# Performance work log

Hardware: AMD Instinct MI355X
Metric: run time of the kernel (lower is better)

Reference implementation:

```python
import jax, jax.numpy as jnp
import numpy as np

SEQ = 2048
D_MODEL = 2048
N_HEAD = 16
D_QK = 128
D_V = 128
THETA = 10000.0


def setup_inputs() -> dict:
    key = jax.random.key(0)
    kx, kq, kk, kv, ko = jax.random.split(key, 5)
    x = jax.random.normal(kx, (SEQ, D_MODEL), dtype=jnp.float32)
    q = jax.random.normal(kq, (N_HEAD, D_MODEL, D_QK), dtype=jnp.float32)
    k = jax.random.normal(kk, (N_HEAD, D_MODEL, D_QK), dtype=jnp.float32)
    v = jax.random.normal(kv, (N_HEAD, D_MODEL, D_V), dtype=jnp.float32)
    o = jax.random.normal(ko, (N_HEAD, D_V, D_MODEL), dtype=jnp.float32)
    theta_factor = jnp.asarray(THETA, dtype=jnp.float32)
    return {"x": x, "q": q, "k": k, "v": v, "o": o, "theta_factor": theta_factor}


def _rope_embed(x, d_qk, theta_factor):
    # x: [..., S, d]. Rotate-half RoPE with frequencies theta^(-i/d_rope),
    # then scale by d_qk^(-1/4) so q.k gets the usual 1/sqrt(d_qk).
    S, d = x.shape[-2], x.shape[-1]
    d_rope = d // 2
    rates = theta_factor ** (-jnp.arange(d_rope, dtype=x.dtype) / d_rope)  # [d_rope]
    ang = jnp.arange(S, dtype=x.dtype)[:, None] * rates[None, :]           # [S, d_rope]
    sin, cos = jnp.sin(ang), jnp.cos(ang)
    x1, x2 = x[..., :d_rope], x[..., d_rope:]
    y = jnp.concatenate([cos * x1 - sin * x2, sin * x1 + cos * x2], axis=-1)
    return y * (d_qk ** -0.25)


def reference(x, q, k, v, o, theta_factor):
    # x: [S, D]; q,k: [H, D, d_qk]; v: [H, D, d_v]; o: [H, d_v, D]
    S = x.shape[0]
    d_qk = q.shape[2]
    qs = jnp.einsum('sd,hde->hse', x, q)   # [H, S, d_qk]
    ks = jnp.einsum('sd,hde->hse', x, k)   # [H, S, d_qk]
    vs = jnp.einsum('sd,hde->hse', x, v)   # [H, S, d_v]
    rq = _rope_embed(qs, d_qk, theta_factor)
    rk = _rope_embed(ks, d_qk, theta_factor)
    scores = jnp.einsum('hse,hte->hst', rq, rk)  # [H, S, S]
    causal = jnp.tril(jnp.ones((S, S), dtype=bool))
    scores = jnp.where(causal[None], scores, -jnp.inf)
    w = jax.nn.softmax(scores, axis=-1)
    y = jnp.einsum('hst,hte->hse', w, vs)        # [H, S, d_v]
    z = jnp.einsum('hse,hed->sd', y, o)          # [S, D] (sum over heads)
    return z
```

## Files before the change

### kernel.cpp

```cpp
#include <hip/hip_runtime.h>
#include <hip/hip_bf16.h>

#define SEQ 2048
#define DM  2048
#define NH  16
#define DE  128
#define DR  64
#define LDT 72
#define LDK 136

typedef __attribute__((ext_vector_type(8))) short bf16x8;
typedef __attribute__((ext_vector_type(4))) float f32x4;

__device__ __forceinline__ unsigned short f2bf(float f) {
  unsigned u = __float_as_uint(f);
  u += 0x7fff + ((u >> 16) & 1);
  return (unsigned short)(u >> 16);
}
__device__ __forceinline__ float bf2f(unsigned short h) {
  return __uint_as_float((unsigned)h << 16);
}

__device__ __forceinline__ void gld16(const unsigned short* g, unsigned short* l) {
  __builtin_amdgcn_global_load_lds(
      (const __attribute__((address_space(1))) unsigned int*)g,
      (__attribute__((address_space(3))) unsigned int*)l, 16, 0, 0);
}

__global__ void k_split(const float* __restrict__ in, unsigned short* __restrict__ hi,
                        unsigned short* __restrict__ lo, int n4) {
  int i = blockIdx.x * blockDim.x + threadIdx.x;
  int stride = gridDim.x * blockDim.x;
  for (int idx = i; idx < n4; idx += stride) {
    float4 v = ((const float4*)in)[idx];
    ushort4 h, l;
    h.x = f2bf(v.x); l.x = f2bf(v.x - bf2f(h.x));
    h.y = f2bf(v.y); l.y = f2bf(v.y - bf2f(h.y));
    h.z = f2bf(v.z); l.z = f2bf(v.z - bf2f(h.z));
    h.w = f2bf(v.w); l.w = f2bf(v.w - bf2f(h.w));
    ((ushort4*)hi)[idx] = h;
    ((ushort4*)lo)[idx] = l;
  }
}

__global__ void k_prep_all(const float* __restrict__ q, const float* __restrict__ k,
                           const float* __restrict__ v, const float* __restrict__ o,
                           unsigned short* __restrict__ wqh, unsigned short* __restrict__ wql,
                           unsigned short* __restrict__ wkh, unsigned short* __restrict__ wkl,
                           unsigned short* __restrict__ wvh, unsigned short* __restrict__ otb) {
  __shared__ float tile[32][33];
  int f = blockIdx.x;
  int tx = threadIdx.x, ty = threadIdx.y;
  if (f < 12288) {
    int z = f >> 8;
    int rem = f & 255;
    int ry = rem >> 2, rx = rem & 3;
    int which = z >> 4, h = z & 15;
    const float* in = (which == 0) ? q : (which == 1) ? k : v;
    size_t bo = (size_t)h * DM * DE;
    int r0 = ry * 32, c0 = rx * 32;
    #pragma unroll
    for (int i = 0; i < 32; i += 8)
      tile[ty + i][tx] = in[bo + (size_t)(r0 + ty + i) * DE + (c0 + tx)];
    __syncthreads();
    #pragma unroll
    for (int i = 0; i < 32; i += 8) {
      float vv = tile[tx][ty + i];
      unsigned short hh = f2bf(vv);
      size_t oidx = bo + (size_t)(c0 + ty + i) * DM + (r0 + tx);
      if (which == 0)      { wqh[oidx] = hh; wql[oidx] = f2bf(vv - bf2f(hh)); }
      else if (which == 1) { wkh[oidx] = hh; wkl[oidx] = f2bf(vv - bf2f(hh)); }
      else                 { wvh[oidx] = hh; }
    }
  } else {
    int rem = f - 12288;
    int ry = rem >> 6, rx = rem & 63;
    int r0 = ry * 32, c0 = rx * 32;
    #pragma unroll
    for (int i = 0; i < 32; i += 8)
      tile[ty + i][tx] = o[(size_t)(r0 + ty + i) * DM + (c0 + tx)];
    __syncthreads();
    #pragma unroll
    for (int i = 0; i < 32; i += 8)
      otb[(size_t)(c0 + ty + i) * DM + (r0 + tx)] = f2bf(tile[tx][ty + i]);
  }
}

__global__ void k_rope_tables(const float* __restrict__ theta_p,
                              float* __restrict__ cost, float* __restrict__ sint) {
  int s = blockIdx.x, j = threadIdx.x;
  float theta = theta_p[0];
  float rate = powf(theta, -(float)j * (1.0f / (float)DR));
  float ang = (float)s * rate;
  cost[s * DR + j] = cosf(ang);
  sint[s * DR + j] = sinf(ang);
}

__launch_bounds__(256)
__global__ void k_projall(const unsigned short* __restrict__ xh, const unsigned short* __restrict__ xl,
                          const unsigned short* __restrict__ wqh, const unsigned short* __restrict__ wql,
                          const unsigned short* __restrict__ wkh, const unsigned short* __restrict__ wkl,
                          const unsigned short* __restrict__ wvh,
                          unsigned short* __restrict__ rqh, unsigned short* __restrict__ rql,
                          unsigned short* __restrict__ rkh, unsigned short* __restrict__ rkl,
                          unsigned short* __restrict__ vstt,
                          const float* __restrict__ cost, const float* __restrict__ sint) {
  __shared__ unsigned short Ahs[2][128 * 32];
  __shared__ unsigned short Als[2][128 * 32];
  __shared__ unsigned short Bhs[2][128 * 32];
  __shared__ unsigned short Bls[2][128 * 32];
  int mt = blockIdx.x;
  int mat = blockIdx.y >> 4, h = blockIdx.y & 15;
  bool split = (mat < 2);
  const unsigned short* wph = (mat == 0 ? wqh : (mat == 1 ? wkh : wvh)) + (size_t)h * DE * DM;
  const unsigned short* wpl = (mat == 0 ? wql : wkl) + (size_t)h * DE * DM;
  int m0 = mt * 128;
  int tid = threadIdx.x, lane = tid & 63, wid = tid >> 6;
  int wr = wid >> 1, wc = wid & 1;

  f32x4 zero = {0.f, 0.f, 0.f, 0.f};
  f32x4 acc[4][4];
  #pragma unroll
  for (int i = 0; i < 4; ++i)
    #pragma unroll
    for (int j = 0; j < 4; ++j) acc[i][j] = zero;

  auto STAGE = [&](int buf, int k0) {
    #pragma unroll
    for (int p = 0; p < 2; ++p) {
      int r = p * 64 + wid * 16 + (lane >> 2);
      int c = ((lane & 3) ^ ((r >> 1) & 3)) * 8;
      int ld = r * 32 + (lane & 3) * 8;
      gld16(&xh[(size_t)(m0 + r) * DM + k0 + c], &Ahs[buf][ld]);
      gld16(&wph[(size_t)r * DM + k0 + c], &Bhs[buf][ld]);
      if (split) {
        gld16(&xl[(size_t)(m0 + r) * DM + k0 + c], &Als[buf][ld]);
        gld16(&wpl[(size_t)r * DM + k0 + c], &Bls[buf][ld]);
      }
    }
  };

  const int NT = DM / 32;
  STAGE(0, 0);
  int cl_ = lane & 15;
  int chunk = lane >> 4;
  #pragma unroll 2
  for (int t = 0; t < NT; ++t) {
    int buf = t & 1;
    __syncthreads();
    if (t + 1 < NT) STAGE(buf ^ 1, (t + 1) * 32);
    bf16x8 ah[4], al[4], bh[4], bl[4];
    #pragma unroll
    for (int mf = 0; mf < 4; ++mf) {
      int row = wr * 64 + mf * 16 + cl_;
      int off = row * 32 + ((chunk ^ ((row >> 1) & 3)) * 8);
      ah[mf] = *(const bf16x8*)&Ahs[buf][off];
      if (split) al[mf] = *(const bf16x8*)&Als[buf][off];
    }
    #pragma unroll
    for (int nf = 0; nf < 4; ++nf) {
      int nfi = wc * 2 + (nf & 1) + (nf >> 1) * 4;
      int row = nfi * 16 + cl_;
      int off = row * 32 + ((chunk ^ ((row >> 1) & 3)) * 8);
      bh[nf] = *(const bf16x8*)&Bhs[buf][off];
      if (split) bl[nf] = *(const bf16x8*)&Bls[buf][off];
    }
    if (split) {
      #pragma unroll
      for (int mf = 0; mf < 4; ++mf)
        #pragma unroll
        for (int nf = 0; nf < 4; ++nf) {
          acc[mf][nf] = __builtin_amdgcn_mfma_f32_16x16x32_bf16(ah[mf], bh[nf], acc[mf][nf], 0, 0, 0);
          acc[mf][nf] = __builtin_amdgcn_mfma_f32_16x16x32_bf16(al[mf], bh[nf], acc[mf][nf], 0, 0, 0);
          acc[mf][nf] = __builtin_amdgcn_mfma_f32_16x16x32_bf16(ah[mf], bl[nf], acc[mf][nf], 0, 0, 0);
        }
    } else {
      #pragma unroll
      for (int mf = 0; mf < 4; ++mf)
        #pragma unroll
        for (int nf = 0; nf < 4; ++nf)
          acc[mf][nf] = __builtin_amdgcn_mfma_f32_16x16x32_bf16(ah[mf], bh[nf], acc[mf][nf], 0, 0, 0);
    }
  }

  int cl = lane & 15, rl = (lane >> 4) * 4;
  if (mat == 2) {
    #pragma unroll
    for (int mf = 0; mf < 4; ++mf)
      #pragma unroll
      for (int nf = 0; nf < 4; ++nf) {
        int nfi = wc * 2 + (nf & 1) + (nf >> 1) * 4;
        #pragma unroll
        for (int j = 0; j < 4; ++j) {
          int s = m0 + wr * 64 + mf * 16 + rl + j;
          int e = nfi * 16 + cl;
          vstt[((size_t)h * DE + e) * SEQ + s] = f2bf(acc[mf][nf][j]);
        }
      }
  } else {
    unsigned short* oh = (mat == 0) ? rqh : rkh;
    unsigned short* ol = (mat == 0) ? rql : rkl;
    const float qsc = 0.2973017787506803f;
    #pragma unroll
    for (int mf = 0; mf < 4; ++mf)
      #pragma unroll
      for (int nf = 0; nf < 2; ++nf)
        #pragma unroll
        for (int j = 0; j < 4; ++j) {
          int s = m0 + wr * 64 + mf * 16 + rl + j;
          int e = wc * 32 + (nf & 1) * 16 + cl;
          float x1 = acc[mf][nf][j];
          float x2 = acc[mf][nf + 2][j];
          float c  = cost[s * DR + e];
          float sn = sint[s * DR + e];
          float v1 = (c * x1 - sn * x2) * qsc;
          float v2 = (sn * x1 + c * x2) * qsc;
          size_t i1 = ((size_t)h * SEQ + s) * DE + e;
          size_t i2 = i1 + DR;
          unsigned short h1 = f2bf(v1), h2 = f2bf(v2);
          oh[i1] = h1; ol[i1] = f2bf(v1 - bf2f(h1));
          oh[i2] = h2; ol[i2] = f2bf(v2 - bf2f(h2));
        }
  }
}

#define LOADKV(t0)                                                        \
  pkh0 = *(const int4*)&Kh[(size_t)((t0) + sk_r     ) * DE + sk_c];       \
  pkh1 = *(const int4*)&Kh[(size_t)((t0) + sk_r + 16) * DE + sk_c];       \
  pkh2 = *(const int4*)&Kh[(size_t)((t0) + sk_r + 32) * DE + sk_c];       \
  pkh3 = *(const int4*)&Kh[(size_t)((t0) + sk_r + 48) * DE + sk_c];       \
  pkl0 = *(const int4*)&Kl[(size_t)((t0) + sk_r     ) * DE + sk_c];       \
  pkl1 = *(const int4*)&Kl[(size_t)((t0) + sk_r + 16) * DE + sk_c];       \
  pkl2 = *(const int4*)&Kl[(size_t)((t0) + sk_r + 32) * DE + sk_c];       \
  pkl3 = *(const int4*)&Kl[(size_t)((t0) + sk_r + 48) * DE + sk_c];       \
  pvv0 = *(const int4*)&Vt[(size_t)(sv_r     ) * SEQ + (t0) + sv_c];      \
  pvv1 = *(const int4*)&Vt[(size_t)(sv_r + 32) * SEQ + (t0) + sv_c];      \
  pvv2 = *(const int4*)&Vt[(size_t)(sv_r + 64) * SEQ + (t0) + sv_c];      \
  pvv3 = *(const int4*)&Vt[(size_t)(sv_r + 96) * SEQ + (t0) + sv_c];

#define STOREKV()                                                         \
  *(int4*)&Khi[(sk_r     ) * LDK + sk_c] = pkh0;                          \
  *(int4*)&Khi[(sk_r + 16) * LDK + sk_c] = pkh1;                          \
  *(int4*)&Khi[(sk_r + 32) * LDK + sk_c] = pkh2;                          \
  *(int4*)&Khi[(sk_r + 48) * LDK + sk_c] = pkh3;                          \
  *(int4*)&Klo[(sk_r     ) * LDK + sk_c] = pkl0;                          \
  *(int4*)&Klo[(sk_r + 16) * LDK + sk_c] = pkl1;                          \
  *(int4*)&Klo[(sk_r + 32) * LDK + sk_c] = pkl2;                          \
  *(int4*)&Klo[(sk_r + 48) * LDK + sk_c] = pkl3;                          \
  *(int4*)&Vtl[(sv_r     ) * LDT + sv_c] = pvv0;                          \
  *(int4*)&Vtl[(sv_r + 32) * LDT + sv_c] = pvv1;                          \
  *(int4*)&Vtl[(sv_r + 64) * LDT + sv_c] = pvv2;                          \
  *(int4*)&Vtl[(sv_r + 96) * LDT + sv_c] = pvv3;

__launch_bounds__(256, 2)
__global__ void k_attn(const unsigned short* __restrict__ rqh, const unsigned short* __restrict__ rql,
                       const unsigned short* __restrict__ rkh, const unsigned short* __restrict__ rkl,
                       const unsigned short* __restrict__ vstt,
                       unsigned short* __restrict__ yb) {
  __shared__ unsigned short Khi[64 * LDK];
  __shared__ unsigned short Klo[64 * LDK];
  __shared__ unsigned short Vtl[128 * LDT];
  __shared__ unsigned short Pl[64 * LDT];
  int bid = blockIdx.x;
  int g = bid >> 4;
  int qt = (g < 16) ? (31 - g) : (g - 16);
  int h  = bid & 15;
  int m0 = qt * 64;
  int tid = threadIdx.x, lane = tid & 63, wid = tid >> 6;
  const unsigned short* Qh = rqh + (size_t)h * SEQ * DE;
  const unsigned short* Ql = rql + (size_t)h * SEQ * DE;
  const unsigned short* Kh = rkh + (size_t)h * SEQ * DE;
  const unsigned short* Kl = rkl + (size_t)h * SEQ * DE;
  const unsigned short* Vt = vstt + (size_t)h * DE * SEQ;
  int cl = lane & 15, hi = lane >> 4;

  bf16x8 qfh[4], qfl[4];
  {
    int qrow = m0 + wid * 16 + cl;
    #pragma unroll
    for (int ks = 0; ks < 4; ++ks) {
      qfh[ks] = *(const bf16x8*)&Qh[(size_t)qrow * DE + ks * 32 + hi * 8];
      qfl[ks] = *(const bf16x8*)&Ql[(size_t)qrow * DE + ks * 32 + hi * 8];
    }
  }

  f32x4 zero = {0.f, 0.f, 0.f, 0.f};
  f32x4 acc[8];
  #pragma unroll
  for (int nf = 0; nf < 8; ++nf) acc[nf] = zero;
  float mrow[4], lrow[4];
  #pragma unroll
  for (int j = 0; j < 4; ++j) { mrow[j] = -3e38f; lrow[j] = 0.f; }

  int sk_r = tid >> 4, sk_c = (tid & 15) * 8;
  int sv_r = tid >> 3, sv_c = (tid & 7) * 8;

  int4 pkh0, pkh1, pkh2, pkh3, pkl0, pkl1, pkl2, pkl3, pvv0, pvv1, pvv2, pvv3;

  int ntiles = qt + 1;
  LOADKV(0)
  for (int t = 0; t < ntiles; ++t) {
    int t0 = t * 64;
    STOREKV()
    __syncthreads();
    if (t + 1 < ntiles) { LOADKV(t0 + 64) }

    f32x4 sacc[4];
    #pragma unroll
    for (int tf = 0; tf < 4; ++tf) sacc[tf] = zero;
    __builtin_amdgcn_s_setprio(1);
    #pragma unroll
    for (int ks = 0; ks < 4; ++ks) {
      int kk = ks * 32 + hi * 8;
      #pragma unroll
      for (int tf = 0; tf < 4; ++tf) {
        int r = (tf * 16 + cl) * LDK + kk;
        bf16x8 bh = *(const bf16x8*)&Khi[r];
        bf16x8 bl = *(const bf16x8*)&Klo[r];
        sacc[tf] = __builtin_amdgcn_mfma_f32_16x16x32_bf16(qfh[ks], bh, sacc[tf], 0, 0, 0);
        sacc[tf] = __builtin_amdgcn_mfma_f32_16x16x32_bf16(qfl[ks], bh, sacc[tf], 0, 0, 0);
        sacc[tf] = __builtin_amdgcn_mfma_f32_16x16x32_bf16(qfh[ks], bl, sacc[tf], 0, 0, 0);
      }
    }
    __builtin_amdgcn_s_setprio(0);
    if (t == ntiles - 1) {
      int sb = m0 + wid * 16 + hi * 4;
      #pragma unroll
      for (int tf = 0; tf < 4; ++tf) {
        int tc = t0 + tf * 16 + cl;
        #pragma unroll
        for (int j = 0; j < 4; ++j)
          if (tc > sb + j) sacc[tf][j] = -3e38f;
      }
    }
    float mxa[4];
    #pragma unroll
    for (int j = 0; j < 4; ++j) {
      float mx = fmaxf(fmaxf(sacc[0][j], sacc[1][j]), fmaxf(sacc[2][j], sacc[3][j]));
      mx = fmaxf(mx, __shfl_xor(mx, 1));
      mx = fmaxf(mx, __shfl_xor(mx, 2));
      mx = fmaxf(mx, __shfl_xor(mx, 4));
      mx = fmaxf(mx, __shfl_xor(mx, 8));
      mxa[j] = mx;
    }
    bool need = (mxa[0] > mrow[0] + 8.f) || (mxa[1] > mrow[1] + 8.f) ||
                (mxa[2] > mrow[2] + 8.f) || (mxa[3] > mrow[3] + 8.f);
    if (__any(need)) {
      #pragma unroll
      for (int j = 0; j < 4; ++j) {
        float mnew = fmaxf(mrow[j], mxa[j]);
        float sc = __expf(mrow[j] - mnew);
        float sum = 0.f;
        #pragma unroll
        for (int tf = 0; tf < 4; ++tf) {
          float p = __expf(sacc[tf][j] - mnew);
          sacc[tf][j] = p;
          sum += p;
        }
        sum += __shfl_xor(sum, 1);
        sum += __shfl_xor(sum, 2);
        sum += __shfl_xor(sum, 4);
        sum += __shfl_xor(sum, 8);
        lrow[j] = lrow[j] * sc + sum;
        mrow[j] = mnew;
        #pragma unroll
        for (int nf = 0; nf < 8; ++nf) acc[nf][j] *= sc;
      }
    } else {
      #pragma unroll
      for (int j = 0; j < 4; ++j) {
        float sum = 0.f;
        #pragma unroll
        for (int tf = 0; tf < 4; ++tf) {
          float p = __expf(sacc[tf][j] - mrow[j]);
          sacc[tf][j] = p;
          sum += p;
        }
        sum += __shfl_xor(sum, 1);
        sum += __shfl_xor(sum, 2);
        sum += __shfl_xor(sum, 4);
        sum += __shfl_xor(sum, 8);
        lrow[j] += sum;
      }
    }
    #pragma unroll
    for (int tf = 0; tf < 4; ++tf)
      #pragma unroll
      for (int j = 0; j < 4; ++j)
        Pl[(wid * 16 + hi * 4 + j) * LDT + tf * 16 + cl] = f2bf(sacc[tf][j]);
    __builtin_amdgcn_s_setprio(1);
    #pragma unroll
    for (int ks = 0; ks < 2; ++ks) {
      int kk = ks * 32 + hi * 8;
      bf16x8 a = *(const bf16x8*)&Pl[(wid * 16 + cl) * LDT + kk];
      #pragma unroll
      for (int nf = 0; nf < 8; ++nf) {
        bf16x8 b = *(const bf16x8*)&Vtl[(nf * 16 + cl) * LDT + kk];
        acc[nf] = __builtin_amdgcn_mfma_f32_16x16x32_bf16(a, b, acc[nf], 0, 0, 0);
      }
    }
    __builtin_amdgcn_s_setprio(0);
    __syncthreads();
  }

  #pragma unroll
  for (int j = 0; j < 4; ++j) {
    float inv = 1.0f / lrow[j];
    #pragma unroll
    for (int nf = 0; nf < 8; ++nf) acc[nf][j] *= inv;
  }
  #pragma unroll
  for (int nf = 0; nf < 8; ++nf)
    #pragma unroll
    for (int j = 0; j < 4; ++j) {
      int s = m0 + wid * 16 + hi * 4 + j;
      int e = nf * 16 + cl;
      yb[(size_t)s * DM + h * DE + e] = f2bf(acc[nf][j]);
    }
}

__launch_bounds__(256)
__global__ void k_out(const unsigned short* __restrict__ yb,
                      const unsigned short* __restrict__ otb,
                      float* __restrict__ z) {
  __shared__ unsigned short Ahs[2][128 * 32];
  __shared__ unsigned short Bhs[2][128 * 32];
  int m0 = blockIdx.x * 128, n0 = blockIdx.y * 128;
  int tid = threadIdx.x, lane = tid & 63, wid = tid >> 6;
  int wr = wid >> 1, wc = wid & 1;
  f32x4 zero = {0.f, 0.f, 0.f, 0.f};
  f32x4 acc[4][4];
  #pragma unroll
  for (int i = 0; i < 4; ++i)
    #pragma unroll
    for (int j = 0; j < 4; ++j) acc[i][j] = zero;

  auto STAGE = [&](int buf, int k0) {
    #pragma unroll
    for (int p = 0; p < 2; ++p) {
      int r = p * 64 + wid * 16 + (lane >> 2);
      int c = ((lane & 3) ^ ((r >> 1) & 3)) * 8;
      int ld = r * 32 + (lane & 3) * 8;
      gld16(&yb[(size_t)(m0 + r) * DM + k0 + c], &Ahs[buf][ld]);
      gld16(&otb[(size_t)(n0 + r) * DM + k0 + c], &Bhs[buf][ld]);
    }
  };

  const int NT = DM / 32;
  STAGE(0, 0);
  int cl_ = lane & 15;
  int chunk = lane >> 4;
  #pragma unroll 2
  for (int t = 0; t < NT; ++t) {
    int buf = t & 1;
    __syncthreads();
    if (t + 1 < NT) STAGE(buf ^ 1, (t + 1) * 32);
    bf16x8 a[4], b[4];
    #pragma unroll
    for (int mf = 0; mf < 4; ++mf) {
      int row = wr * 64 + mf * 16 + cl_;
      a[mf] = *(const bf16x8*)&Ahs[buf][row * 32 + ((chunk ^ ((row >> 1) & 3)) * 8)];
    }
    #pragma unroll
    for (int nf = 0; nf < 4; ++nf) {
      int nfi = wc * 2 + (nf & 1) + (nf >> 1) * 4;
      int row = nfi * 16 + cl_;
      b[nf] = *(const bf16x8*)&Bhs[buf][row * 32 + ((chunk ^ ((row >> 1) & 3)) * 8)];
    }
    #pragma unroll
    for (int mf = 0; mf < 4; ++mf)
      #pragma unroll
      for (int nf = 0; nf < 4; ++nf)
        acc[mf][nf] = __builtin_amdgcn_mfma_f32_16x16x32_bf16(a[mf], b[nf], acc[mf][nf], 0, 0, 0);
  }
  int cl = lane & 15, rl = (lane >> 4) * 4;
  #pragma unroll
  for (int mf = 0; mf < 4; ++mf)
    #pragma unroll
    for (int nf = 0; nf < 4; ++nf) {
      int nfi = wc * 2 + (nf & 1) + (nf >> 1) * 4;
      #pragma unroll
      for (int j = 0; j < 4; ++j) {
        int s = m0 + wr * 64 + mf * 16 + rl + j;
        int d = n0 + nfi * 16 + cl;
        z[(size_t)s * DM + d] = acc[mf][nf][j];
      }
    }
}

extern "C" void kernel_launch(void* const* d_in, const int* in_sizes, int n_in,
                              void* d_out, int out_size, void* d_ws, size_t ws_size,
                              hipStream_t stream) {
  const float* x  = (const float*)d_in[0];
  const float* q  = (const float*)d_in[1];
  const float* k  = (const float*)d_in[2];
  const float* v  = (const float*)d_in[3];
  const float* o  = (const float*)d_in[4];
  const float* th = (const float*)d_in[5];
  float* z = (float*)d_out;
  char* ws = (char*)d_ws;
  const size_t MB = 1024 * 1024;
  unsigned short* xh  = (unsigned short*)(ws);
  unsigned short* xl  = (unsigned short*)(ws + 8 * MB);
  unsigned short* wqh = (unsigned short*)(ws + 16 * MB);
  unsigned short* wql = (unsigned short*)(ws + 24 * MB);
  unsigned short* wkh = (unsigned short*)(ws + 32 * MB);
  unsigned short* wkl = (unsigned short*)(ws + 40 * MB);
  unsigned short* wvh = (unsigned short*)(ws + 48 * MB);
  unsigned short* rqh = (unsigned short*)(ws + 56 * MB);
  unsigned short* rql = (unsigned short*)(ws + 64 * MB);
  unsigned short* rkh = (unsigned short*)(ws + 72 * MB);
  unsigned short* rkl = (unsigned short*)(ws + 80 * MB);
  unsigned short* vst = (unsigned short*)(ws + 88 * MB);
  float* cost = (float*)(ws + 96 * MB);
  float* sint = (float*)(ws + 96 * MB + 512 * 1024);
  unsigned short* otb = (unsigned short*)(ws + 98 * MB);
  unsigned short* yb  = (unsigned short*)(ws + 16 * MB);

  dim3 tb(32, 8);
  k_rope_tables<<<SEQ, DR, 0, stream>>>(th, cost, sint);
  k_split<<<2048, 256, 0, stream>>>(x, xh, xl, SEQ * DM / 4);
  k_prep_all<<<16384, tb, 0, stream>>>(q, k, v, o, wqh, wql, wkh, wkl, wvh, otb);
  k_projall<<<dim3(16, 48), 256, 0, stream>>>(xh, xl, wqh, wql, wkh, wkl, wvh,
                                              rqh, rql, rkh, rkl, vst, cost, sint);
  k_attn<<<512, 256, 0, stream>>>(rqh, rql, rkh, rkl, vst, yb);
  k_out<<<dim3(16, 16), 256, 0, stream>>>(yb, otb, z);
}
```

Before: 312.3 us.

## Shrink attention tiles to 32 rows with 2-wave blocks and interleave heads

The attention kernel now uses 32-query by 32-key tiles with 128-thread blocks (two waves) and launches twice as many blocks. Shared-memory buffers and strides are resized to match, and the head index is permuted across block IDs. The goal is better load balance and occupancy across CUs for the causal triangular workload. In exchange, each key/value byte is reused by fewer query rows, so more tile loads and barriers are needed per unit of work.

New measurement: 324.9 us. +4.0%, slower.

```diff
diff --git a/kernel.cpp b/kernel.cpp
--- a/kernel.cpp
+++ b/kernel.cpp
@@ -6,8 +6,9 @@
 #define NH  16
 #define DE  128
 #define DR  64
-#define LDT 72
 #define LDK 136
+#define LDV 36
+#define LDP 36
 
 typedef __attribute__((ext_vector_type(8))) short bf16x8;
 typedef __attribute__((ext_vector_type(4))) float f32x4;
@@ -226,13 +227,13 @@
 
 #define LOADKV(t0)                                                        \
   pkh0 = *(const int4*)&Kh[(size_t)((t0) + sk_r     ) * DE + sk_c];       \
-  pkh1 = *(const int4*)&Kh[(size_t)((t0) + sk_r + 16) * DE + sk_c];       \
-  pkh2 = *(const int4*)&Kh[(size_t)((t0) + sk_r + 32) * DE + sk_c];       \
-  pkh3 = *(const int4*)&Kh[(size_t)((t0) + sk_r + 48) * DE + sk_c];       \
+  pkh1 = *(const int4*)&Kh[(size_t)((t0) + sk_r +  8) * DE + sk_c];       \
+  pkh2 = *(const int4*)&Kh[(size_t)((t0) + sk_r + 16) * DE + sk_c];       \
+  pkh3 = *(const int4*)&Kh[(size_t)((t0) + sk_r + 24) * DE + sk_c];       \
   pkl0 = *(const int4*)&Kl[(size_t)((t0) + sk_r     ) * DE + sk_c];       \
-  pkl1 = *(const int4*)&Kl[(size_t)((t0) + sk_r + 16) * DE + sk_c];       \
-  pkl2 = *(const int4*)&Kl[(size_t)((t0) + sk_r + 32) * DE + sk_c];       \
-  pkl3 = *(const int4*)&Kl[(size_t)((t0) + sk_r + 48) * DE + sk_c];       \
+  pkl1 = *(const int4*)&Kl[(size_t)((t0) + sk_r +  8) * DE + sk_c];       \
+  pkl2 = *(const int4*)&Kl[(size_t)((t0) + sk_r + 16) * DE + sk_c];       \
+  pkl3 = *(const int4*)&Kl[(size_t)((t0) + sk_r + 24) * DE + sk_c];       \
   pvv0 = *(const int4*)&Vt[(size_t)(sv_r     ) * SEQ + (t0) + sv_c];      \
   pvv1 = *(const int4*)&Vt[(size_t)(sv_r + 32) * SEQ + (t0) + sv_c];      \
   pvv2 = *(const int4*)&Vt[(size_t)(sv_r + 64) * SEQ + (t0) + sv_c];      \
@@ -240,32 +241,32 @@
 
 #define STOREKV()                                                         \
   *(int4*)&Khi[(sk_r     ) * LDK + sk_c] = pkh0;                          \
-  *(int4*)&Khi[(sk_r + 16) * LDK + sk_c] = pkh1;                          \
-  *(int4*)&Khi[(sk_r + 32) * LDK + sk_c] = pkh2;                          \
-  *(int4*)&Khi[(sk_r + 48) * LDK + sk_c] = pkh3;                          \
+  *(int4*)&Khi[(sk_r +  8) * LDK + sk_c] = pkh1;                          \
+  *(int4*)&Khi[(sk_r + 16) * LDK + sk_c] = pkh2;                          \
+  *(int4*)&Khi[(sk_r + 24) * LDK + sk_c] = pkh3;                          \
   *(int4*)&Klo[(sk_r     ) * LDK + sk_c] = pkl0;                          \
-  *(int4*)&Klo[(sk_r + 16) * LDK + sk_c] = pkl1;                          \
-  *(int4*)&Klo[(sk_r + 32) * LDK + sk_c] = pkl2;                          \
-  *(int4*)&Klo[(sk_r + 48) * LDK + sk_c] = pkl3;                          \
-  *(int4*)&Vtl[(sv_r     ) * LDT + sv_c] = pvv0;                          \
-  *(int4*)&Vtl[(sv_r + 32) * LDT + sv_c] = pvv1;                          \
-  *(int4*)&Vtl[(sv_r + 64) * LDT + sv_c] = pvv2;                          \
-  *(int4*)&Vtl[(sv_r + 96) * LDT + sv_c] = pvv3;
-
-__launch_bounds__(256, 2)
+  *(int4*)&Klo[(sk_r +  8) * LDK + sk_c] = pkl1;                          \
+  *(int4*)&Klo[(sk_r + 16) * LDK + sk_c] = pkl2;                          \
+  *(int4*)&Klo[(sk_r + 24) * LDK + sk_c] = pkl3;                          \
+  *(int4*)&Vtl[(sv_r     ) * LDV + sv_c] = pvv0;                          \
+  *(int4*)&Vtl[(sv_r + 32) * LDV + sv_c] = pvv1;                          \
+  *(int4*)&Vtl[(sv_r + 64) * LDV + sv_c] = pvv2;                          \
+  *(int4*)&Vtl[(sv_r + 96) * LDV + sv_c] = pvv3;
+
+__launch_bounds__(128, 2)
 __global__ void k_attn(const unsigned short* __restrict__ rqh, const unsigned short* __restrict__ rql,
                        const unsigned short* __restrict__ rkh, const unsigned short* __restrict__ rkl,
                        const unsigned short* __restrict__ vstt,
                        unsigned short* __restrict__ yb) {
-  __shared__ unsigned short Khi[64 * LDK];
-  __shared__ unsigned short Klo[64 * LDK];
-  __shared__ unsigned short Vtl[128 * LDT];
-  __shared__ unsigned short Pl[64 * LDT];
+  __shared__ unsigned short Khi[32 * LDK];
+  __shared__ unsigned short Klo[32 * LDK];
+  __shared__ unsigned short Vtl[128 * LDV];
+  __shared__ unsigned short Pl[32 * LDP];
   int bid = blockIdx.x;
+  int h = ((bid & 7) << 1) | ((bid >> 3) & 1);
   int g = bid >> 4;
-  int qt = (g < 16) ? (31 - g) : (g - 16);
-  int h  = bid & 15;
-  int m0 = qt * 64;
+  int qt = (g < 32) ? (63 - g) : (g - 32);
+  int m0 = qt * 32;
   int tid = threadIdx.x, lane = tid & 63, wid = tid >> 6;
   const unsigned short* Qh = rqh + (size_t)h * SEQ * DE;
   const unsigned short* Ql = rql + (size_t)h * SEQ * DE;
@@ -293,27 +294,27 @@
   for (int j = 0; j < 4; ++j) { mrow[j] = -3e38f; lrow[j] = 0.f; }
 
   int sk_r = tid >> 4, sk_c = (tid & 15) * 8;
-  int sv_r = tid >> 3, sv_c = (tid & 7) * 8;
+  int sv_r = tid >> 2, sv_c = (tid & 3) * 8;
 
   int4 pkh0, pkh1, pkh2, pkh3, pkl0, pkl1, pkl2, pkl3, pvv0, pvv1, pvv2, pvv3;
 
   int ntiles = qt + 1;
   LOADKV(0)
   for (int t = 0; t < ntiles; ++t) {
-    int t0 = t * 64;
+    int t0 = t * 32;
     STOREKV()
     __syncthreads();
-    if (t + 1 < ntiles) { LOADKV(t0 + 64) }
-
-    f32x4 sacc[4];
-    #pragma unroll
-    for (int tf = 0; tf < 4; ++tf) sacc[tf] = zero;
+    if (t + 1 < ntiles) { LOADKV(t0 + 32) }
+
+    f32x4 sacc[2];
+    #pragma unroll
+    for (int tf = 0; tf < 2; ++tf) sacc[tf] = zero;
     __builtin_amdgcn_s_setprio(1);
     #pragma unroll
     for (int ks = 0; ks < 4; ++ks) {
       int kk = ks * 32 + hi * 8;
       #pragma unroll
-      for (int tf = 0; tf < 4; ++tf) {
+      for (int tf = 0; tf < 2; ++tf) {
         int r = (tf * 16 + cl) * LDK + kk;
         bf16x8 bh = *(const bf16x8*)&Khi[r];
         bf16x8 bl = *(const bf16x8*)&Klo[r];
@@ -326,7 +327,7 @@
     if (t == ntiles - 1) {
       int sb = m0 + wid * 16 + hi * 4;
       #pragma unroll
-      for (int tf = 0; tf < 4; ++tf) {
+      for (int tf = 0; tf < 2; ++tf) {
         int tc = t0 + tf * 16 + cl;
         #pragma unroll
         for (int j = 0; j < 4; ++j)
@@ -336,7 +337,7 @@
     float mxa[4];
     #pragma unroll
     for (int j = 0; j < 4; ++j) {
-      float mx = fmaxf(fmaxf(sacc[0][j], sacc[1][j]), fmaxf(sacc[2][j], sacc[3][j]));
+      float mx = fmaxf(sacc[0][j], sacc[1][j]);
       mx = fmaxf(mx, __shfl_xor(mx, 1));
       mx = fmaxf(mx, __shfl_xor(mx, 2));
       mx = fmaxf(mx, __shfl_xor(mx, 4));
@@ -352,7 +353,7 @@
         float sc = __expf(mrow[j] - mnew);
         float sum = 0.f;
         #pragma unroll
-        for (int tf = 0; tf < 4; ++tf) {
+        for (int tf = 0; tf < 2; ++tf) {
           float p = __expf(sacc[tf][j] - mnew);
           sacc[tf][j] = p;
           sum += p;
@@ -371,7 +372,7 @@
       for (int j = 0; j < 4; ++j) {
         float sum = 0.f;
         #pragma unroll
-        for (int tf = 0; tf < 4; ++tf) {
+        for (int tf = 0; tf < 2; ++tf) {
           float p = __expf(sacc[tf][j] - mrow[j]);
           sacc[tf][j] = p;
           sum += p;
@@ -384,18 +385,17 @@
       }
     }
     #pragma unroll
-    for (int tf = 0; tf < 4; ++tf)
+    for (int tf = 0; tf < 2; ++tf)
       #pragma unroll
       for (int j = 0; j < 4; ++j)
-        Pl[(wid * 16 + hi * 4 + j) * LDT + tf * 16 + cl] = f2bf(sacc[tf][j]);
+        Pl[(wid * 16 + hi * 4 + j) * LDP + tf * 16 + cl] = f2bf(sacc[tf][j]);
     __builtin_amdgcn_s_setprio(1);
-    #pragma unroll
-    for (int ks = 0; ks < 2; ++ks) {
-      int kk = ks * 32 + hi * 8;
-      bf16x8 a = *(const bf16x8*)&Pl[(wid * 16 + cl) * LDT + kk];
+    {
+      int kk = hi * 8;
+      bf16x8 a = *(const bf16x8*)&Pl[(wid * 16 + cl) * LDP + kk];
       #pragma unroll
       for (int nf = 0; nf < 8; ++nf) {
-        bf16x8 b = *(const bf16x8*)&Vtl[(nf * 16 + cl) * LDT + kk];
+        bf16x8 b = *(const bf16x8*)&Vtl[(nf * 16 + cl) * LDV + kk];
         acc[nf] = __builtin_amdgcn_mfma_f32_16x16x32_bf16(a, b, acc[nf], 0, 0, 0);
       }
     }
@@ -523,6 +523,6 @@
   k_prep_all<<<16384, tb, 0, stream>>>(q, k, v, o, wqh, wql, wkh, wkl, wvh, otb);
   k_projall<<<dim3(16, 48), 256, 0, stream>>>(xh, xl, wqh, wql, wkh, wkl, wvh,
                                               rqh, rql, rkh, rkl, vst, cost, sint);
-  k_attn<<<512, 256, 0, stream>>>(rqh, rql, rkh, rkl, vst, yb);
+  k_attn<<<1024, 128, 0, stream>>>(rqh, rql, rkh, rkl, vst, yb);
   k_out<<<dim3(16, 16), 256, 0, stream>>>(yb, otb, z);
 }
```
